# Optimization experiments

Hardware: AMD Instinct MI355X
Metric: run time of the kernel (lower is better)

The kernel has to match this reference:

```python
import jax, jax.numpy as jnp
import numpy as np

EPS = 1e-12  # torch F.normalize eps


def _l2norm(x, axis):
    return x / jnp.maximum(jnp.linalg.norm(x, axis=axis, keepdims=True), EPS)


def setup_inputs() -> dict:
    key = jax.random.key(0)
    ks = jax.random.split(key, 8)
    B, N, D_in, H, K, D_out = 16, 1024, 1024, 512, 64, 1024
    return {
        "input_data": jax.random.normal(ks[0], (B, N, D_in), dtype=jnp.float32),
        "fc1_w": jax.random.normal(ks[1], (H, D_in), dtype=jnp.float32) * 0.02,
        "fc1_b": jax.random.normal(ks[2], (H,), dtype=jnp.float32) * 0.02,
        "conv_w": jax.random.normal(ks[3], (K, H), dtype=jnp.float32) * 0.1,
        "conv_b": jax.random.normal(ks[4], (K,), dtype=jnp.float32) * 0.1,
        "centroids": jax.random.normal(ks[5], (K, H), dtype=jnp.float32),
        "fc2_w": jax.random.normal(ks[6], (D_out, K * H), dtype=jnp.float32) * 0.01,
        "fc2_b": jax.random.normal(ks[7], (D_out,), dtype=jnp.float32) * 0.01,
    }


def reference(input_data, fc1_w, fc1_b, conv_w, conv_b, centroids, fc2_w, fc2_b):
    # fc1 + relu: [B, N, H]
    h = jax.nn.relu(jnp.einsum('bnd,hd->bnh', input_data, fc1_w) + fc1_b)
    # NetVLAD input layout: [B, H, N] (the (N,1) spatial dims collapse to N)
    x = jnp.swapaxes(h, 1, 2)
    # normalize descriptors across feature dim (F.normalize(x, p=2, dim=1))
    xn = _l2norm(x, axis=1)
    # 1x1-conv soft assignment -> softmax over clusters: [B, K, N]
    logits = jnp.einsum('kh,bhn->bkn', conv_w, xn) + conv_b[None, :, None]
    a = jax.nn.softmax(logits, axis=1)
    # vlad_{bkh} = sum_n a_{bkn} (xn_{bhn} - c_{kh})  (fused, no [B,K,H,N] tensor)
    vlad = jnp.einsum('bkn,bhn->bkh', a, xn) - a.sum(axis=-1)[:, :, None] * centroids[None]
    vlad = _l2norm(vlad, axis=2)              # intra-normalization
    vlad = vlad.reshape(vlad.shape[0], -1)    # [B, K*H]
    vlad = _l2norm(vlad, axis=1)              # global L2 norm
    # fc2 + relu: [B, out_dim]
    return jax.nn.relu(vlad @ fc2_w.T + fc2_b)
```

## Files before the change

kernel.cpp:

```cpp
#include <hip/hip_runtime.h>
#include <hip/hip_bf16.h>

typedef __bf16  bf16x8 __attribute__((ext_vector_type(8)));
typedef float   f32x4  __attribute__((ext_vector_type(4)));

#define DEV __device__ __forceinline__

DEV ushort f2b(float f){
  union { float f; unsigned u; } c; c.f = f;
  unsigned u = c.u;
  unsigned r = (u + 0x7FFFu + ((u >> 16) & 1u)) >> 16;
  return (ushort)r;
}
DEV float b2f(ushort h){
  union { unsigned u; float f; } c; c.u = ((unsigned)h) << 16;
  return c.f;
}
DEV float wredsum(float v){
  #pragma unroll
  for(int o = 32; o > 0; o >>= 1) v += __shfl_xor(v, o, 64);
  return v;
}
DEV float wredmax(float v){
  #pragma unroll
  for(int o = 32; o > 0; o >>= 1) v = fmaxf(v, __shfl_xor(v, o, 64));
  return v;
}
DEV void gload_lds16(const void* g, void* l){
  __builtin_amdgcn_global_load_lds(
      (const __attribute__((address_space(1))) void*)g,
      (__attribute__((address_space(3))) void*)l,
      16, 0, 0);
}
DEV bf16x8 cvt8(float4 a0, float4 a1){
  bf16x8 t;
  t[0]=(__bf16)a0.x; t[1]=(__bf16)a0.y; t[2]=(__bf16)a0.z; t[3]=(__bf16)a0.w;
  t[4]=(__bf16)a1.x; t[5]=(__bf16)a1.y; t[6]=(__bf16)a1.z; t[7]=(__bf16)a1.w;
  return t;
}

__global__ void prep(const float* __restrict__ W1, const float* __restrict__ CW,
                     const float* __restrict__ CB,
                     ushort* __restrict__ W1b, ushort* __restrict__ CWb,
                     float* __restrict__ CBp){
  int bid = blockIdx.x, tid = threadIdx.x;
  if(bid < 512){
    int i = bid * 256 + tid;
    float4 f = ((const float4*)W1)[i];
    ushort4 o; o.x = f2b(f.x); o.y = f2b(f.y); o.z = f2b(f.z); o.w = f2b(f.w);
    ((ushort4*)W1b)[i] = o;
  } else if(bid < 640){
    int i = (bid - 512) * 256 + tid;
    CWb[i] = f2b(CW[i]);
  } else {
    if(tid < 128) CBp[tid] = (tid < 64) ? CB[tid] : 0.0f;
  }
}

__global__ __launch_bounds__(512) void fc1sm(
    const float* __restrict__ A, const ushort* __restrict__ B,
    const float* __restrict__ bias, const ushort* __restrict__ CWb,
    const float* __restrict__ CBp, ushort* __restrict__ XNT,
    ushort* __restrict__ AThi, ushort* __restrict__ ATlo)
{
  const int K = 1024;
  __shared__ __align__(16) char smem[81920];
  const int tid = threadIdx.x, lane = tid & 63, wid = tid >> 6;
  const int bm0 = blockIdx.x * 64;
  const int wr = (wid >> 2) * 32;
  const int wc = (wid & 3) * 128;
  const int wcol = wid & 3;
  const int arow = lane & 15;
  const int khalf = lane >> 4;

  const int srow = tid >> 3;
  const int sseg = tid & 7;
  const char* asrc = (const char*)A + (size_t)(bm0 + srow) * 4096
                     + (sseg ^ (srow & 7)) * 16;
  const ushort* bg = B + (size_t)(tid >> 2) * K + ((tid & 3) ^ ((tid >> 3) & 3)) * 8;

  f32x4 acc[2][8];
  #pragma unroll
  for(int i = 0; i < 2; i++)
    #pragma unroll
    for(int j = 0; j < 8; j++) acc[i][j] = (f32x4){0.f, 0.f, 0.f, 0.f};

#define STAGE_F1N(buf, kb) do { \
    gload_lds16(asrc + (kb), smem + (buf) * 8192 + tid * 16); \
    const ushort* bs_ = bg + ((kb) >> 2); \
    char* bd_ = smem + 16384 + (buf) * 32768 + tid * 16; \
    gload_lds16(bs_,           bd_); \
    gload_lds16(bs_ + 128 * K, bd_ + 8192); \
    gload_lds16(bs_ + 256 * K, bd_ + 16384); \
    gload_lds16(bs_ + 384 * K, bd_ + 24576); \
  } while(0)

  STAGE_F1N(0, 0);

  #pragma unroll
  for(int ks = 0; ks < 32; ++ks){
    const int cur = ks & 1;
    if(ks + 1 < 32){
      STAGE_F1N(cur ^ 1, (ks + 1) * 128);
      asm volatile("s_waitcnt vmcnt(5)" ::: "memory");
    } else {
      asm volatile("s_waitcnt vmcnt(0)" ::: "memory");
    }
    __builtin_amdgcn_s_barrier();
    __builtin_amdgcn_sched_barrier(0);
    bf16x8 af[2], bfr[8];
    #pragma unroll
    for(int mi = 0; mi < 2; mi++){
      int r = wr + mi * 16 + arow;
      const char* base = smem + cur * 8192 + r * 128;
      float4 a0 = *(const float4*)(base + (((khalf * 2)     ^ (r & 7)) * 16));
      float4 a1 = *(const float4*)(base + (((khalf * 2 + 1) ^ (r & 7)) * 16));
      af[mi] = cvt8(a0, a1);
    }
    #pragma unroll
    for(int ni = 0; ni < 8; ni++){
      int r = wc + ni * 16 + arow;
      bfr[ni] = *(const bf16x8*)(smem + 16384 + cur * 32768
                                 + r * 64 + ((khalf ^ ((r >> 1) & 3)) * 16));
    }
    #pragma unroll
    for(int mi = 0; mi < 2; mi++)
      #pragma unroll
      for(int ni = 0; ni < 8; ni++)
        acc[mi][ni] = __builtin_amdgcn_mfma_f32_16x16x32_bf16(af[mi], bfr[ni], acc[mi][ni], 0, 0, 0);
    __builtin_amdgcn_sched_barrier(0);
    __builtin_amdgcn_s_barrier();
  }
#undef STAGE_F1N

  ushort* xnm     = (ushort*)smem;
  float*  ssq_pA  = (float*)(smem + 66560);
  float*  scale_A = (float*)(smem + 67584);

  float bv[8];
  #pragma unroll
  for(int ni = 0; ni < 8; ni++) bv[ni] = bias[wc + ni * 16 + arow];
  float p[2][4];
  #pragma unroll
  for(int mi = 0; mi < 2; mi++)
    #pragma unroll
    for(int i = 0; i < 4; i++){
      float s = 0.f;
      #pragma unroll
      for(int ni = 0; ni < 8; ni++){
        float v = fmaxf(acc[mi][ni][i] + bv[ni], 0.f);
        acc[mi][ni][i] = v;
        s += v * v;
      }
      p[mi][i] = s;
    }
  #pragma unroll
  for(int o = 1; o < 16; o <<= 1)
    #pragma unroll
    for(int mi = 0; mi < 2; mi++)
      #pragma unroll
      for(int i = 0; i < 4; i++)
        p[mi][i] += __shfl_xor(p[mi][i], o, 64);
  if(arow == 0){
    #pragma unroll
    for(int mi = 0; mi < 2; mi++)
      #pragma unroll
      for(int i = 0; i < 4; i++)
        ssq_pA[wcol * 64 + wr + mi * 16 + khalf * 4 + i] = p[mi][i];
  }
  __syncthreads();
  if(tid < 64){
    float s = ssq_pA[tid] + ssq_pA[64 + tid] + ssq_pA[128 + tid] + ssq_pA[192 + tid];
    scale_A[tid] = 1.0f / fmaxf(sqrtf(s), 1e-12f);
  }
  __syncthreads();

  #pragma unroll
  for(int mi = 0; mi < 2; mi++)
    #pragma unroll
    for(int i = 0; i < 4; i++){
      int rt = wr + mi * 16 + khalf * 4 + i;
      float sc = scale_A[rt];
      #pragma unroll
      for(int ni = 0; ni < 8; ni++){
        int h = wc + ni * 16 + arow;
        xnm[rt * 520 + h] = f2b(acc[mi][ni][i] * sc);
      }
    }
  __syncthreads();

  const int bb = bm0 >> 10, n0b = bm0 & 1023;

  if(wid < 4){
    const int t = wid, c = arow;
    f32x4 lg[4];
    #pragma unroll
    for(int kf = 0; kf < 4; kf++) lg[kf] = (f32x4){0.f,0.f,0.f,0.f};
    const ushort* cw0 = CWb + (size_t)c * 512 + khalf * 8;
    const char*   xb0 = (const char*)xnm + (t * 16 + c) * 1040 + khalf * 16;
    #pragma unroll
    for(int s = 0; s < 16; ++s){
      bf16x8 xb = *(const bf16x8*)(xb0 + s * 64);
      #pragma unroll
      for(int kf = 0; kf < 4; kf++){
        bf16x8 cwf = *(const bf16x8*)(cw0 + (size_t)kf * 16 * 512 + s * 32);
        lg[kf] = __builtin_amdgcn_mfma_f32_16x16x32_bf16(cwf, xb, lg[kf], 0, 0, 0);
      }
    }
    float l[4][4];
    float m = -3.4e38f;
    #pragma unroll
    for(int kf = 0; kf < 4; kf++)
      #pragma unroll
      for(int i = 0; i < 4; i++){
        l[kf][i] = lg[kf][i] + CBp[kf * 16 + khalf * 4 + i];
        m = fmaxf(m, l[kf][i]);
      }
    m = fmaxf(m, __shfl_xor(m, 16, 64));
    m = fmaxf(m, __shfl_xor(m, 32, 64));
    float s = 0.f;
    #pragma unroll
    for(int kf = 0; kf < 4; kf++)
      #pragma unroll
      for(int i = 0; i < 4; i++){
        l[kf][i] = __expf(l[kf][i] - m);
        s += l[kf][i];
      }
    s += __shfl_xor(s, 16, 64);
    s += __shfl_xor(s, 32, 64);
    float inv = 1.0f / s;
    #pragma unroll
    for(int kf = 0; kf < 4; kf++)
      #pragma unroll
      for(int i = 0; i < 4; i++){
        float a = l[kf][i] * inv;
        ushort hi = f2b(a);
        float lo = a - b2f(hi);
        int k = kf * 16 + khalf * 4 + i;
        size_t idx = ((size_t)bb * 64 + k) * 1024 + n0b + t * 16 + c;
        AThi[idx] = hi;
        ATlo[idx] = f2b(lo);
      }
  } else {
    #pragma unroll
    for(int rep = 0; rep < 2; rep++){
      int h = (tid - 256) + rep * 256;
      unsigned tmp[32];
      #pragma unroll
      for(int j = 0; j < 32; j++){
        unsigned lo = xnm[(2 * j)     * 520 + h];
        unsigned hi = xnm[(2 * j + 1) * 520 + h];
        tmp[j] = lo | (hi << 16);
      }
      ushort* dst = XNT + ((size_t)bb * 512 + h) * 1024 + n0b;
      #pragma unroll
      for(int u = 0; u < 8; u++){
        uint4 w; w.x = tmp[u*4]; w.y = tmp[u*4+1]; w.z = tmp[u*4+2]; w.w = tmp[u*4+3];
        *(uint4*)(dst + u * 8) = w;
      }
    }
  }
}

__global__ __launch_bounds__(512) void vlad_mfma(
    const ushort* __restrict__ AThi, const ushort* __restrict__ ATlo,
    const ushort* __restrict__ XNT, const float* __restrict__ cent,
    ushort* __restrict__ vlb, float* __restrict__ ssq)
{
  __shared__ __align__(16) ushort Ah[2][16 * 32];
  __shared__ __align__(16) ushort Al[2][16 * 32];
  __shared__ __align__(16) ushort Xs[2][512 * 32];
  __shared__ float red[8][16];
  __shared__ float scale_s[16], ssqn_s[16];
  const int tid = threadIdx.x, lane = tid & 63, wid = tid >> 6;
  const int b = blockIdx.x, kg = blockIdx.y;
  const int k0 = kg * 16;
  const int hw = wid;
  const int arow = lane & 15, khalf = lane >> 4;

  const int xslot = (tid & 3) ^ ((tid >> 3) & 3);
  const ushort* xg = XNT + ((size_t)b * 512 + (tid >> 2)) * 1024 + xslot * 8;
  const int aslot = (lane & 3) ^ ((lane >> 3) & 3);
  const ushort* ahg = AThi + ((size_t)b * 64 + k0 + (lane >> 2)) * 1024 + aslot * 8;
  const ushort* alg = ATlo + ((size_t)b * 64 + k0 + (lane >> 2)) * 1024 + aslot * 8;

  f32x4 acc[4];
  #pragma unroll
  for(int i = 0; i < 4; i++) acc[i] = (f32x4){0.f, 0.f, 0.f, 0.f};
  f32x4 asum = (f32x4){0.f, 0.f, 0.f, 0.f};
  bf16x8 ones;
  #pragma unroll
  for(int j = 0; j < 8; j++) ones[j] = (__bf16)1.0f;

#define STAGE_VL(buf, n0v) do { \
    char* xd = (char*)&Xs[buf][0] + tid * 16; \
    gload_lds16(xg + (n0v),                xd); \
    gload_lds16(xg + (n0v) + 128 * 1024,   xd + 8192); \
    gload_lds16(xg + (n0v) + 256 * 1024,   xd + 16384); \
    gload_lds16(xg + (n0v) + 384 * 1024,   xd + 24576); \
    if(wid == 0)      gload_lds16(ahg + (n0v), (char*)&Ah[buf][0] + lane * 16); \
    else if(wid == 1) gload_lds16(alg + (n0v), (char*)&Al[buf][0] + lane * 16); \
  } while(0)

  STAGE_VL(0, 0);
  __syncthreads();

  int cur = 0;
  for(int ks = 0; ks < 32; ++ks){
    if(ks + 1 < 32) STAGE_VL(cur ^ 1, (ks + 1) * 32);
    bf16x8 ah, al, bfr[4];
    {
      int sl = khalf ^ ((arow >> 1) & 3);
      ah = *(const bf16x8*)&Ah[cur][arow * 32 + sl * 8];
      al = *(const bf16x8*)&Al[cur][arow * 32 + sl * 8];
    }
    #pragma unroll
    for(int ni = 0; ni < 4; ni++){
      int r = hw * 64 + ni * 16 + arow;
      bfr[ni] = *(const bf16x8*)&Xs[cur][r * 32 + ((khalf ^ ((r >> 1) & 3)) * 8)];
    }
    asum = __builtin_amdgcn_mfma_f32_16x16x32_bf16(ah, ones, asum, 0, 0, 0);
    asum = __builtin_amdgcn_mfma_f32_16x16x32_bf16(al, ones, asum, 0, 0, 0);
    #pragma unroll
    for(int ni = 0; ni < 4; ni++){
      acc[ni] = __builtin_amdgcn_mfma_f32_16x16x32_bf16(ah, bfr[ni], acc[ni], 0, 0, 0);
      acc[ni] = __builtin_amdgcn_mfma_f32_16x16x32_bf16(al, bfr[ni], acc[ni], 0, 0, 0);
    }
    __syncthreads();
    cur ^= 1;
  }
#undef STAGE_VL

  float vl[4][4];
  #pragma unroll
  for(int ni = 0; ni < 4; ni++)
    #pragma unroll
    for(int i = 0; i < 4; i++){
      int r_ = (lane >> 4) * 4 + i;
      int h = hw * 64 + ni * 16 + (lane & 15);
      vl[ni][i] = acc[ni][i] - asum[i] * cent[(size_t)(k0 + r_) * 512 + h];
    }
  float sq[4];
  #pragma unroll
  for(int i = 0; i < 4; i++){
    float s = 0.f;
    #pragma unroll
    for(int ni = 0; ni < 4; ni++) s += vl[ni][i] * vl[ni][i];
    sq[i] = s;
  }
  #pragma unroll
  for(int o = 1; o < 16; o <<= 1)
    #pragma unroll
    for(int i = 0; i < 4; i++) sq[i] += __shfl_xor(sq[i], o, 64);
  if((lane & 15) == 0){
    #pragma unroll
    for(int i = 0; i < 4; i++) red[hw][(lane >> 4) * 4 + i] = sq[i];
  }
  __syncthreads();
  if(tid < 16){
    float s = 0.f;
    #pragma unroll
    for(int w = 0; w < 8; w++) s += red[w][tid];
    float sc = 1.0f / fmaxf(sqrtf(s), 1e-12f);
    scale_s[tid] = sc;
    ssqn_s[tid] = s * sc * sc;
  }
  __syncthreads();
  if(tid < 4)
    ssq[b * 16 + kg * 4 + tid] = ssqn_s[tid * 4] + ssqn_s[tid * 4 + 1]
                               + ssqn_s[tid * 4 + 2] + ssqn_s[tid * 4 + 3];
  #pragma unroll
  for(int ni = 0; ni < 4; ni++)
    #pragma unroll
    for(int i = 0; i < 4; i++){
      int r_ = (lane >> 4) * 4 + i;
      int h = hw * 64 + ni * 16 + (lane & 15);
      vlb[(size_t)b * 32768 + (size_t)(k0 + r_) * 512 + h] = f2b(vl[ni][i] * scale_s[r_]);
    }
}

__global__ __launch_bounds__(256) void fc2_mfma(const float* __restrict__ W,
                                                const ushort* __restrict__ vlb,
                                                float* __restrict__ part){
  __shared__ __align__(16) float Bs[2][128 * 32];
  const int tid = threadIdx.x, lane = tid & 63, wid = tid >> 6;
  const int c0 = blockIdx.x * 128;
  const int kc = blockIdx.y;
  const size_t kbase = (size_t)kc * 256;

  const int srow = tid >> 3;
  const int seg  = tid & 7;
  f32x4 acc0 = (f32x4){0.f,0.f,0.f,0.f};
  f32x4 acc1 = (f32x4){0.f,0.f,0.f,0.f};

  const int arow = lane & 15;
  const int khalf = lane >> 4;
  const int cRow0 = wid * 32 + (lane & 15);
  const int cRow1 = cRow0 + 16;

  #pragma unroll
  for(int pass = 0; pass < 4; ++pass){
    int row = pass * 32 + srow;
    const char* src = (const char*)W + (size_t)(c0 + row) * 131072
                      + kbase * 4 + ((seg ^ (row & 7)) * 16);
    gload_lds16(src, (char*)&Bs[0][0] + row * 128 + seg * 16);
  }
  __syncthreads();

  int cur = 0;
  for(int ks = 0; ks < 8; ++ks){
    if(ks + 1 < 8){
      #pragma unroll
      for(int pass = 0; pass < 4; ++pass){
        int row = pass * 32 + srow;
        const char* src = (const char*)W + (size_t)(c0 + row) * 131072
                          + (kbase + (ks + 1) * 32) * 4 + ((seg ^ (row & 7)) * 16);
        gload_lds16(src, (char*)&Bs[cur ^ 1][0] + row * 128 + seg * 16);
      }
    }
    bf16x8 af = *(const bf16x8*)((const char*)vlb + (size_t)arow * 65536
                                 + (kbase + ks * 32 + khalf * 8) * 2);
    int t0 = khalf * 2;
    const char* bsc = (const char*)&Bs[cur][0];
    float4 b00 = *(const float4*)(bsc + cRow0 * 128 + ((t0     ^ (cRow0 & 7)) * 16));
    float4 b01 = *(const float4*)(bsc + cRow0 * 128 + (((t0+1) ^ (cRow0 & 7)) * 16));
    float4 b10 = *(const float4*)(bsc + cRow1 * 128 + ((t0     ^ (cRow1 & 7)) * 16));
    float4 b11 = *(const float4*)(bsc + cRow1 * 128 + (((t0+1) ^ (cRow1 & 7)) * 16));
    bf16x8 bf0 = cvt8(b00, b01);
    bf16x8 bf1 = cvt8(b10, b11);

    acc0 = __builtin_amdgcn_mfma_f32_16x16x32_bf16(af, bf0, acc0, 0, 0, 0);
    acc1 = __builtin_amdgcn_mfma_f32_16x16x32_bf16(af, bf1, acc1, 0, 0, 0);
    __syncthreads();
    cur ^= 1;
  }

  #pragma unroll
  for(int i = 0; i < 4; ++i){
    int b = (lane >> 4) * 4 + i;
    int d0 = c0 + wid * 32 + (lane & 15);
    part[((size_t)kc * 16 + b) * 1024 + d0]      = acc0[i];
    part[((size_t)kc * 16 + b) * 1024 + d0 + 16] = acc1[i];
  }
}

__global__ __launch_bounds__(256) void fin(const float* __restrict__ part, const float* __restrict__ ssq,
                                           const float* __restrict__ b2, float* __restrict__ out){
  __shared__ float red[4][64];
  int lane = threadIdx.x & 63, wq = threadIdx.x >> 6;
  int o = blockIdx.x * 64 + lane;
  int b = o >> 10, d = o & 1023;
  float s = 0;
  #pragma unroll
  for(int i = 0; i < 32; i++){
    int t = wq * 32 + i;
    s += part[((size_t)t * 16 + b) * 1024 + d];
  }
  red[wq][lane] = s;
  __syncthreads();
  if(wq == 0){
    float g = 0;
    #pragma unroll
    for(int kg = 0; kg < 16; kg++) g += ssq[b * 16 + kg];
    float gsv = 1.0f / fmaxf(sqrtf(g), 1e-12f);
    float tot = red[0][lane] + red[1][lane] + red[2][lane] + red[3][lane];
    out[o] = fmaxf(gsv * tot + b2[d], 0.0f);
  }
}

extern "C" void kernel_launch(void* const* d_in, const int* in_sizes, int n_in,
                              void* d_out, int out_size, void* d_ws, size_t ws_size,
                              hipStream_t stream){
  const float* X    = (const float*)d_in[0];
  const float* W1   = (const float*)d_in[1];
  const float* B1   = (const float*)d_in[2];
  const float* CW   = (const float*)d_in[3];
  const float* CB   = (const float*)d_in[4];
  const float* CENT = (const float*)d_in[5];
  const float* W2   = (const float*)d_in[6];
  const float* B2   = (const float*)d_in[7];
  float* out = (float*)d_out;
  char* ws = (char*)d_ws;

  ushort* W1b  = (ushort*)(ws + 0);
  ushort* CWb  = (ushort*)(ws + 1048576);
  float*  CBp  = (float*) (ws + 1114112);
  ushort* XNT  = (ushort*)(ws + 1114624);
  ushort* AThi = (ushort*)(ws + 17891840);
  ushort* ATlo = (ushort*)(ws + 19988992);
  ushort* VLb  = (ushort*)(ws + 22086144);
  float*  SSQ  = (float*) (ws + 23134720);
  float*  PART = (float*) (ws + 23135744);

  prep<<<641, 256, 0, stream>>>(W1, CW, CB, W1b, CWb, CBp);
  fc1sm<<<256, 512, 0, stream>>>(X, W1b, B1, CWb, CBp, XNT, AThi, ATlo);
  vlad_mfma<<<dim3(16, 4), 512, 0, stream>>>(AThi, ATlo, XNT, CENT, VLb, SSQ);
  fc2_mfma<<<dim3(8, 128), 256, 0, stream>>>(W2, VLb, PART);
  fin<<<256, 256, 0, stream>>>(PART, SSQ, B2, out);
}
```

Measured before the change: 108.5 us.

## Give each wave private LDS staging in fc1 GEMM to drop block barriers

The fc1 GEMM main loop moves from a block-shared, double-buffered LDS tile to per-wave private LDS regions. Each wave now loads its own 32-row A slice and double-buffered 128-column B slices, so the per-iteration block barriers go away. Waves synchronise only through vmcnt and lgkmcnt waits, and the next loads are issued right after the fragments are read into registers. The trade-off is that LDS use doubles to 160 KB per block, which limits residency to one block per CU. Global loads are also duplicated: each A row is fetched by 4 waves and each B row by 2, which adds L2 traffic.

Measured after the change: 115.7 us. 1.07x slower.

```diff
diff --git a/kernel.cpp b/kernel.cpp
--- a/kernel.cpp
+++ b/kernel.cpp
@@ -15,16 +15,6 @@
 DEV float b2f(ushort h){
   union { unsigned u; float f; } c; c.u = ((unsigned)h) << 16;
   return c.f;
-}
-DEV float wredsum(float v){
-  #pragma unroll
-  for(int o = 32; o > 0; o >>= 1) v += __shfl_xor(v, o, 64);
-  return v;
-}
-DEV float wredmax(float v){
-  #pragma unroll
-  for(int o = 32; o > 0; o >>= 1) v = fmaxf(v, __shfl_xor(v, o, 64));
-  return v;
 }
 DEV void gload_lds16(const void* g, void* l){
   __builtin_amdgcn_global_load_lds(
@@ -64,7 +54,7 @@
     ushort* __restrict__ AThi, ushort* __restrict__ ATlo)
 {
   const int K = 1024;
-  __shared__ __align__(16) char smem[81920];
+  __shared__ __align__(16) char smem[163840];
   const int tid = threadIdx.x, lane = tid & 63, wid = tid >> 6;
   const int bm0 = blockIdx.x * 64;
   const int wr = (wid >> 2) * 32;
@@ -73,11 +63,12 @@
   const int arow = lane & 15;
   const int khalf = lane >> 4;
 
-  const int srow = tid >> 3;
-  const int sseg = tid & 7;
-  const char* asrc = (const char*)A + (size_t)(bm0 + srow) * 4096
-                     + (sseg ^ (srow & 7)) * 16;
-  const ushort* bg = B + (size_t)(tid >> 2) * K + ((tid & 3) ^ ((tid >> 3) & 3)) * 8;
+  char* wbase = smem + wid * 20480;
+
+  const char* asrcw = (const char*)A + (size_t)(bm0 + wr + (lane >> 3)) * 4096
+                      + ((lane & 7) ^ ((lane >> 3) & 7)) * 16;
+  const ushort* bsrcw = B + (size_t)(wc + (lane >> 2)) * K
+                      + ((lane & 3) ^ ((lane >> 3) & 3)) * 8;
 
   f32x4 acc[2][8];
   #pragma unroll
@@ -85,53 +76,57 @@
     #pragma unroll
     for(int j = 0; j < 8; j++) acc[i][j] = (f32x4){0.f, 0.f, 0.f, 0.f};
 
-#define STAGE_F1N(buf, kb) do { \
-    gload_lds16(asrc + (kb), smem + (buf) * 8192 + tid * 16); \
-    const ushort* bs_ = bg + ((kb) >> 2); \
-    char* bd_ = smem + 16384 + (buf) * 32768 + tid * 16; \
-    gload_lds16(bs_,           bd_); \
-    gload_lds16(bs_ + 128 * K, bd_ + 8192); \
-    gload_lds16(bs_ + 256 * K, bd_ + 16384); \
-    gload_lds16(bs_ + 384 * K, bd_ + 24576); \
+#define STAGE_A(kb) do { \
+    _Pragma("unroll") \
+    for(int j_ = 0; j_ < 4; j_++) \
+      gload_lds16(asrcw + (size_t)j_ * 8 * 4096 + (kb), \
+                  wbase + j_ * 1024 + lane * 16); \
   } while(0)
-
-  STAGE_F1N(0, 0);
+#define STAGE_B(buf, ke) do { \
+    _Pragma("unroll") \
+    for(int j_ = 0; j_ < 8; j_++) \
+      gload_lds16(bsrcw + (size_t)j_ * 16 * K + (ke), \
+                  wbase + 4096 + (buf) * 8192 + j_ * 1024 + lane * 16); \
+  } while(0)
+
+  STAGE_B(0, 0);
+  STAGE_A(0);
+  STAGE_B(1, 32);
 
   #pragma unroll
   for(int ks = 0; ks < 32; ++ks){
-    const int cur = ks & 1;
-    if(ks + 1 < 32){
-      STAGE_F1N(cur ^ 1, (ks + 1) * 128);
-      asm volatile("s_waitcnt vmcnt(5)" ::: "memory");
-    } else {
-      asm volatile("s_waitcnt vmcnt(0)" ::: "memory");
-    }
-    __builtin_amdgcn_s_barrier();
+    if(ks < 31) asm volatile("s_waitcnt vmcnt(8)" ::: "memory");
+    else        asm volatile("s_waitcnt vmcnt(0)" ::: "memory");
     __builtin_amdgcn_sched_barrier(0);
+
+    const char* bbuf = wbase + 4096 + (ks & 1) * 8192;
     bf16x8 af[2], bfr[8];
     #pragma unroll
     for(int mi = 0; mi < 2; mi++){
-      int r = wr + mi * 16 + arow;
-      const char* base = smem + cur * 8192 + r * 128;
+      int r = mi * 16 + arow;
+      const char* base = wbase + r * 128;
       float4 a0 = *(const float4*)(base + (((khalf * 2)     ^ (r & 7)) * 16));
       float4 a1 = *(const float4*)(base + (((khalf * 2 + 1) ^ (r & 7)) * 16));
       af[mi] = cvt8(a0, a1);
     }
     #pragma unroll
     for(int ni = 0; ni < 8; ni++){
-      int r = wc + ni * 16 + arow;
-      bfr[ni] = *(const bf16x8*)(smem + 16384 + cur * 32768
-                                 + r * 64 + ((khalf ^ ((r >> 1) & 3)) * 16));
-    }
+      int r = ni * 16 + arow;
+      bfr[ni] = *(const bf16x8*)(bbuf + r * 64 + ((khalf ^ ((r >> 1) & 3)) * 16));
+    }
+    asm volatile("s_waitcnt lgkmcnt(0)" ::: "memory");
+    __builtin_amdgcn_sched_barrier(0);
+    if(ks + 1 < 32) STAGE_A((ks + 1) * 128);
+    if(ks + 2 < 32) STAGE_B(ks & 1, (ks + 2) * 32);
+
     #pragma unroll
     for(int mi = 0; mi < 2; mi++)
       #pragma unroll
       for(int ni = 0; ni < 8; ni++)
         acc[mi][ni] = __builtin_amdgcn_mfma_f32_16x16x32_bf16(af[mi], bfr[ni], acc[mi][ni], 0, 0, 0);
-    __builtin_amdgcn_sched_barrier(0);
-    __builtin_amdgcn_s_barrier();
-  }
-#undef STAGE_F1N
+  }
+#undef STAGE_A
+#undef STAGE_B
 
   ushort* xnm     = (ushort*)smem;
   float*  ssq_pA  = (float*)(smem + 66560);
@@ -161,6 +156,9 @@
       #pragma unroll
       for(int i = 0; i < 4; i++)
         p[mi][i] += __shfl_xor(p[mi][i], o, 64);
+
+  __syncthreads();
+
   if(arow == 0){
     #pragma unroll
     for(int mi = 0; mi < 2; mi++)
```
